# Performance work log

Hardware: AMD Instinct MI355X
Metric: run time of the kernel (lower is better)

Reference implementation:

```python
import jax, jax.numpy as jnp
import numpy as np

N_HEAD = 16
D_HEAD = 64
N_GROUPS = 4
D_EMBED = 1024
ROPE_N = 32
B, T = 2, 2048


def apply_rope(x, cos, sin):
    # x: (..., T, ROPE_N); cos/sin: (T, ROPE_N) broadcast over leading dims
    h = x.shape[-1]
    x1, x2 = x[..., : h // 2], x[..., h // 2 :]
    rotated = jnp.concatenate((-x2, x1), axis=-1)
    return (x * cos + rotated * sin).astype(x.dtype)


def setup_inputs() -> dict:
    key = jax.random.key(0)
    k1, k2, k3, k4, k5 = jax.random.split(key, 5)
    return {
        "x": jax.random.normal(k1, (B, T, D_EMBED), dtype=jnp.float32),
        "cos": jax.random.uniform(k2, (T, ROPE_N), dtype=jnp.float32),
        "sin": jax.random.uniform(k3, (T, ROPE_N), dtype=jnp.float32),
        "mask": jnp.ones((B, T), dtype=bool),  # unused by the original forward (passes None to SDPA)
        "Wqkv": jax.random.normal(k4, (D_EMBED, (N_HEAD + 2 * N_GROUPS) * D_HEAD), dtype=jnp.float32) * 0.02,
        "Wout": jax.random.normal(k5, (N_HEAD * D_HEAD, D_EMBED), dtype=jnp.float32) * 0.02,
    }


def reference(x, cos, sin, mask, Wqkv, Wout):
    Bv, Tv, _ = x.shape
    q_per_kv = N_HEAD // N_GROUPS  # 4
    total_qkv = q_per_kv + 2       # 6

    qkv = jnp.einsum("btc,cf->btf", x, Wqkv)  # (B, T, 1536)
    qkv = qkv.reshape(Bv, Tv, N_GROUPS, total_qkv, D_HEAD)
    qkv = jnp.transpose(qkv, (0, 2, 3, 1, 4))  # (B, G, total_qkv, T, d)

    q = qkv[:, :, :q_per_kv]           # (B, G, q_per_kv, T, d)
    k = qkv[:, :, q_per_kv : q_per_kv + 1]  # (B, G, 1, T, d)
    v = qkv[:, :, q_per_kv + 1 :]           # (B, G, 1, T, d)

    # GQA expand (1 < groups < heads)
    k = jnp.broadcast_to(k, (Bv, N_GROUPS, q_per_kv, Tv, D_HEAD))
    v = jnp.broadcast_to(v, (Bv, N_GROUPS, q_per_kv, Tv, D_HEAD))

    q = q.reshape(Bv, N_HEAD, Tv, D_HEAD)
    k = k.reshape(Bv, N_HEAD, Tv, D_HEAD)
    v = v.reshape(Bv, N_HEAD, Tv, D_HEAD)

    # partial RoPE on the first ROPE_N dims of each head
    q = jnp.concatenate((apply_rope(q[..., :ROPE_N], cos, sin), q[..., ROPE_N:]), axis=-1)
    k = jnp.concatenate((apply_rope(k[..., :ROPE_N], cos, sin), k[..., ROPE_N:]), axis=-1)

    scale = 1.0 / np.sqrt(D_HEAD).astype(np.float32)
    scores = jnp.einsum("bhtd,bhsd->bhts", q, k) * scale
    attn = jax.nn.softmax(scores, axis=-1)
    y = jnp.einsum("bhts,bhsd->bhtd", attn, v)   # (B, H, T, d)
    y = jnp.transpose(y, (0, 2, 1, 3)).reshape(Bv, Tv, N_HEAD * D_HEAD)
    return jnp.einsum("btf,fc->btc", y, Wout)
```

## Files before the change

kernel.cpp:

```cpp
#include <hip/hip_runtime.h>
#include <hip/hip_bf16.h>
#include <math.h>

#define BATCH   2
#define TSEQ    2048
#define DEMBED  1024
#define NHEAD   16
#define DHEAD   64
#define NGROUP  4
#define ROPEN   32
#define FQKV    1536
#define MROWS   (BATCH*TSEQ)

typedef __attribute__((ext_vector_type(8))) short short8;
typedef __attribute__((ext_vector_type(4))) float floatx4;

__device__ __forceinline__ void split_pack8(const float* f, uint4& h4, uint4& l4) {
    uint u[8], lu[8];
    #pragma unroll
    for (int j = 0; j < 8; ++j) {
        u[j] = __float_as_uint(f[j]);
        float lf = f[j] - __uint_as_float(u[j] & 0xffff0000u);
        lu[j] = __float_as_uint(lf);
    }
    h4.x = __builtin_amdgcn_perm(u[1], u[0], 0x07060302u);
    h4.y = __builtin_amdgcn_perm(u[3], u[2], 0x07060302u);
    h4.z = __builtin_amdgcn_perm(u[5], u[4], 0x07060302u);
    h4.w = __builtin_amdgcn_perm(u[7], u[6], 0x07060302u);
    l4.x = __builtin_amdgcn_perm(lu[1], lu[0], 0x07060302u);
    l4.y = __builtin_amdgcn_perm(lu[3], lu[2], 0x07060302u);
    l4.z = __builtin_amdgcn_perm(lu[5], lu[4], 0x07060302u);
    l4.w = __builtin_amdgcn_perm(lu[7], lu[6], 0x07060302u);
}

__device__ __forceinline__ void rtn_pack8(const float* f, uint4& h4) {
    uint t[8];
    #pragma unroll
    for (int j = 0; j < 8; ++j)
        t[j] = __float_as_uint(f[j]) + 0x8000u;
    h4.x = __builtin_amdgcn_perm(t[1], t[0], 0x07060302u);
    h4.y = __builtin_amdgcn_perm(t[3], t[2], 0x07060302u);
    h4.z = __builtin_amdgcn_perm(t[5], t[4], 0x07060302u);
    h4.w = __builtin_amdgcn_perm(t[7], t[6], 0x07060302u);
}

__device__ __forceinline__ uint pk_bf16x2(float f0, float f1) {
    uint u0 = __float_as_uint(f0) + 0x8000u;
    uint u1 = __float_as_uint(f1) + 0x8000u;
    return __builtin_amdgcn_perm(u1, u0, 0x07060302u);
}

__device__ __forceinline__ float fast_exp2(float x) {
    float r;
    asm("v_exp_f32 %0, %1" : "=v"(r) : "v"(x));
    return r;
}

__device__ __forceinline__ void lds_async16(void* lds, const void* gp) {
    __builtin_amdgcn_global_load_lds(
        (const __attribute__((address_space(1))) unsigned int*)gp,
        (__attribute__((address_space(3))) unsigned int*)lds,
        16, 0, 0);
}


__global__ __launch_bounds__(256) void conv_xy(const float* __restrict__ in,
                                               char* __restrict__ img) {
    const int tid = threadIdx.x;
    const int c   = blockIdx.x & 15;
    const int mt  = blockIdx.x >> 4;
    const int r    = tid >> 1;
    const int half = tid & 1;

    const float* src = in + (size_t)(mt*128 + r)*1024 + c*64 + half*32;
    float f[32];
    #pragma unroll
    for (int u = 0; u < 8; ++u)
        *(float4*)(f + 4*u) = *(const float4*)(src + 4*u);

    char* tile = img + ((size_t)(mt*16 + c)) * 32768;
    #pragma unroll
    for (int cc = 0; cc < 4; ++cc) {
        uint4 h4, l4;
        split_pack8(f + cc*8, h4, l4);
        int j    = half*4 + cc;
        int phys = j ^ (r & 7);
        *(uint4*)(tile + r*128 + phys*16)         = h4;
        *(uint4*)(tile + 16384 + r*128 + phys*16) = l4;
    }
}

__global__ __launch_bounds__(256) void conv_w(const float* __restrict__ W,
                                              int N,
                                              char* __restrict__ img) {
    __shared__ float Lf[64][132];
    const int tid = threadIdx.x;
    const int c   = blockIdx.x;
    const int nt  = blockIdx.y;

    {
        const int kk = tid >> 2;
        const int nc = (tid & 3) * 32;
        const float* src = W + (size_t)(c*64 + kk)*N + nt*128 + nc;
        #pragma unroll
        for (int u = 0; u < 8; ++u)
            *(float4*)(&Lf[kk][nc + 4*u]) = *(const float4*)(src + 4*u);
    }
    __syncthreads();

    char* tile = img + ((size_t)(nt*16 + c)) * 32768;
    #pragma unroll
    for (int rep = 0; rep < 4; ++rep) {
        int idx = rep*256 + tid;
        int n = idx & 127;
        int j = idx >> 7;
        float v[8];
        #pragma unroll
        for (int i = 0; i < 8; ++i) v[i] = Lf[j*8 + i][n];
        uint4 h4, l4;
        split_pack8(v, h4, l4);
        int phys = j ^ (n & 7);
        *(uint4*)(tile + n*128 + phys*16)         = h4;
        *(uint4*)(tile + 16384 + n*128 + phys*16) = l4;
    }
}

struct GemmAcc { floatx4 a[4][4]; };

__device__ __forceinline__ void gemm_mfma_core(const char* __restrict__ Aimg,
                                               const char* __restrict__ Bimg,
                                               char* smem, int mt, int nt,
                                               int tid, GemmAcc& G) {
    const int wv = tid >> 6;
    const int wm = wv & 1, wn = wv >> 1;
    const int lane = tid & 63;
    const int qd = lane >> 4, cl = lane & 15;
    const int wslot = (tid & 192) * 16;

    #pragma unroll
    for (int tm = 0; tm < 4; ++tm)
        #pragma unroll
        for (int tn = 0; tn < 4; ++tn)
            G.a[tm][tn] = (floatx4){0.f, 0.f, 0.f, 0.f};

    for (int c = 0; c < 16; ++c) {
        __syncthreads();
        {
            const uint4* gA = (const uint4*)(Aimg + ((size_t)(mt*16 + c)) * 32768) + tid;
            const uint4* gB = (const uint4*)(Bimg + ((size_t)(nt*16 + c)) * 32768) + tid;
            #pragma unroll
            for (int j = 0; j < 8; ++j) {
                lds_async16(smem + j*4096 + wslot,         gA + j*256);
                lds_async16(smem + 32768 + j*4096 + wslot, gB + j*256);
            }
        }
        __syncthreads();

        #pragma unroll
        for (int s = 0; s < 2; ++s) {
            const int phys = ((s*4 + qd) ^ (cl & 7)) * 16;
            short8 ah[4], al[4], bh[4], bl[4];
            #pragma unroll
            for (int tt = 0; tt < 4; ++tt) {
                const int rA = wm*64 + 16*tt + cl;
                ah[tt] = *(const short8*)(smem + rA*128 + phys);
                al[tt] = *(const short8*)(smem + 16384 + rA*128 + phys);
                const int rB = wn*64 + 16*tt + cl;
                bh[tt] = *(const short8*)(smem + 32768 + rB*128 + phys);
                bl[tt] = *(const short8*)(smem + 49152 + rB*128 + phys);
            }
            #pragma unroll
            for (int tm = 0; tm < 4; ++tm)
                #pragma unroll
                for (int tn = 0; tn < 4; ++tn) {
                    G.a[tm][tn] = __builtin_amdgcn_mfma_f32_16x16x32_bf16(ah[tm], bh[tn], G.a[tm][tn], 0, 0, 0);
                    G.a[tm][tn] = __builtin_amdgcn_mfma_f32_16x16x32_bf16(al[tm], bh[tn], G.a[tm][tn], 0, 0, 0);
                    G.a[tm][tn] = __builtin_amdgcn_mfma_f32_16x16x32_bf16(ah[tm], bl[tn], G.a[tm][tn], 0, 0, 0);
                }
        }
    }
}

__global__ __launch_bounds__(256, 2) void gemm_qkv_mfma(const char* __restrict__ Aimg,
                                                        const char* __restrict__ Bimg,
                                                        const float* __restrict__ cosp,
                                                        const float* __restrict__ sinp,
                                                        float* __restrict__ Qf,
                                                        ushort* __restrict__ Kimg,
                                                        ushort* __restrict__ Vimg) {
    __shared__ __align__(16) char smem[68608];
    const int tid = threadIdx.x;
    const int nt = blockIdx.x, mt = blockIdx.y;

    GemmAcc G;
    gemm_mfma_core(Aimg, Bimg, smem, mt, nt, tid, G);

    const int wv = tid >> 6;
    const int wm = wv & 1, wn = wv >> 1;
    const int lane = tid & 63;
    const int qd = lane >> 4, cl = lane & 15;

    const int slice = nt*2 + wn;
    const int g  = slice / 6;
    const int jj = slice % 6;
    const int b  = mt >> 4;

    if (jj != 5) {
        #pragma unroll
        for (int tm = 0; tm < 4; ++tm)
            #pragma unroll
            for (int r = 0; r < 4; ++r) {
                int m = mt*128 + wm*64 + 16*tm + 4*qd + r;
                int t = m & 2047;
                float c1 = cosp[t*ROPEN + cl],      s1 = sinp[t*ROPEN + cl];
                float c2 = cosp[t*ROPEN + 16 + cl], s2 = sinp[t*ROPEN + 16 + cl];
                float x1 = G.a[tm][0][r], x2 = G.a[tm][1][r];
                G.a[tm][0][r] = x1*c1 - x2*s1;
                G.a[tm][1][r] = x2*c2 + x1*s2;
            }
    }

    if (jj < 4) {
        #pragma unroll
        for (int tm = 0; tm < 4; ++tm)
            #pragma unroll
            for (int tn = 0; tn < 4; ++tn)
                #pragma unroll
                for (int r = 0; r < 4; ++r) {
                    int m = mt*128 + wm*64 + 16*tm + 4*qd + r;
                    Qf[(size_t)m*1024 + (g*4 + jj)*64 + 16*tn + cl] = G.a[tm][tn][r];
                }
    } else {
        float* Lw = (float*)(smem + wv*17152);
        __syncthreads();
        #pragma unroll
        for (int tm = 0; tm < 4; ++tm)
            #pragma unroll
            for (int tn = 0; tn < 4; ++tn)
                #pragma unroll
                for (int r = 0; r < 4; ++r)
                    Lw[(16*tm + 4*qd + r)*67 + 16*tn + cl] = G.a[tm][tn][r];
        __syncthreads();

        const int cloc = (mt & 15)*2 + wm;
        ushort* img = ((jj == 4) ? Kimg : Vimg)
                      + (size_t)(b*4 + g)*262144 + (size_t)cloc*8192;
        if (jj == 4) {
            const int rr = lane;
            float f[8];
            #pragma unroll
            for (int ch = 0; ch < 8; ++ch) {
                *(float4*)f       = *(const float4*)(&Lw[rr*67 + ch*8]);
                *(float4*)(f + 4) = *(const float4*)(&Lw[rr*67 + ch*8 + 4]);
                uint4 h4, l4;
                split_pack8(f, h4, l4);
                int phys = ch ^ (rr & 7);
                *(uint4*)(img + rr*64 + phys*8)        = h4;
                *(uint4*)(img + 4096 + rr*64 + phys*8) = l4;
            }
        } else {
            const int d = lane;
            float f[8];
            #pragma unroll
            for (int ch = 0; ch < 8; ++ch) {
                #pragma unroll
                for (int i = 0; i < 8; ++i) f[i] = Lw[(ch*8 + i)*67 + d];
                uint4 h4;
                rtn_pack8(f, h4);
                int phys = ch ^ (d & 7);
                *(uint4*)(img + d*64 + phys*8) = h4;
            }
        }
    }
}

__global__ __launch_bounds__(256, 2) void gemm_out_mfma(const char* __restrict__ Aimg,
                                                        const char* __restrict__ Bimg,
                                                        float* __restrict__ C) {
    __shared__ __align__(16) char smem[49152];
    const int tid = threadIdx.x;
    const int nt = blockIdx.x, mt = blockIdx.y;

    const int wv = tid >> 6;
    const int wm = wv & 1, wn = wv >> 1;
    const int lane = tid & 63;
    const int qd = lane >> 4, cl = lane & 15;
    const int wslot = (tid & 192) * 16;

    floatx4 acc[2][4];
    #pragma unroll
    for (int tm = 0; tm < 2; ++tm)
        #pragma unroll
        for (int tn = 0; tn < 4; ++tn)
            acc[tm][tn] = (floatx4){0.f, 0.f, 0.f, 0.f};

    for (int c = 0; c < 16; ++c) {
        __syncthreads();
        {
            const char* sA = Aimg + ((size_t)((mt >> 1)*16 + c))*32768
                                  + (mt & 1)*8192 + (size_t)tid*16;
            const char* sB = Bimg + ((size_t)(nt*16 + c))*32768 + (size_t)tid*16;
            lds_async16(smem + wslot,          sA);
            lds_async16(smem + 4096  + wslot,  sA + 4096);
            lds_async16(smem + 8192  + wslot,  sA + 16384);
            lds_async16(smem + 12288 + wslot,  sA + 16384 + 4096);
            #pragma unroll
            for (int j = 0; j < 4; ++j) {
                lds_async16(smem + 16384 + j*4096 + wslot, sB + j*4096);
                lds_async16(smem + 32768 + j*4096 + wslot, sB + 16384 + j*4096);
            }
        }
        __syncthreads();

        #pragma unroll
        for (int s = 0; s < 2; ++s) {
            const int phys = ((s*4 + qd) ^ (cl & 7)) * 16;
            short8 ah[2], al[2], bh[4], bl[4];
            #pragma unroll
            for (int tt = 0; tt < 2; ++tt) {
                const int rA = wm*32 + 16*tt + cl;
                ah[tt] = *(const short8*)(smem + rA*128 + phys);
                al[tt] = *(const short8*)(smem + 8192 + rA*128 + phys);
            }
            #pragma unroll
            for (int tt = 0; tt < 4; ++tt) {
                const int rB = wn*64 + 16*tt + cl;
                bh[tt] = *(const short8*)(smem + 16384 + rB*128 + phys);
                bl[tt] = *(const short8*)(smem + 32768 + rB*128 + phys);
            }
            #pragma unroll
            for (int tm = 0; tm < 2; ++tm)
                #pragma unroll
                for (int tn = 0; tn < 4; ++tn) {
                    acc[tm][tn] = __builtin_amdgcn_mfma_f32_16x16x32_bf16(ah[tm], bh[tn], acc[tm][tn], 0, 0, 0);
                    acc[tm][tn] = __builtin_amdgcn_mfma_f32_16x16x32_bf16(al[tm], bh[tn], acc[tm][tn], 0, 0, 0);
                    acc[tm][tn] = __builtin_amdgcn_mfma_f32_16x16x32_bf16(ah[tm], bl[tn], acc[tm][tn], 0, 0, 0);
                }
        }
    }

    #pragma unroll
    for (int tm = 0; tm < 2; ++tm)
        #pragma unroll
        for (int tn = 0; tn < 4; ++tn)
            #pragma unroll
            for (int r = 0; r < 4; ++r) {
                int m = mt*64 + wm*32 + 16*tm + 4*qd + r;
                int n = nt*128 + wn*64 + 16*tn + cl;
                C[(size_t)m*1024 + n] = acc[tm][tn][r];
            }
}

__global__ __launch_bounds__(256, 4) void attn10(const float* __restrict__ Qf,
                                                 const char* __restrict__ Kimg,
                                                 const char* __restrict__ Vimg,
                                                 char* __restrict__ Yimg) {
    __shared__ __align__(16) char smem[37888];
    uint* Pp32 = (uint*)(smem + 32768);

    const int tid  = threadIdx.x;
    const int wv   = tid >> 6;
    const int lane = tid & 63;
    const int qd   = lane >> 4;
    const int cl   = lane & 15;

    const int bg    = blockIdx.x & 7;
    const int inner = blockIdx.x >> 3;
    const int hj    = inner >> 5;
    const int qt    = inner & 31;
    const int b = bg >> 2, g = bg & 3;
    const int h = g*4 + hj;

    short8 qh[2], ql[2];
    {
        const float* qp = Qf + (size_t)(b*2048 + qt*64 + wv*16 + cl)*1024
                             + h*64 + 8*qd;
        #pragma unroll
        for (int s = 0; s < 2; ++s) {
            float f[8];
            *(float4*)f       = *(const float4*)(qp + 32*s);
            *(float4*)(f + 4) = *(const float4*)(qp + 32*s + 4);
            #pragma unroll
            for (int i = 0; i < 8; ++i) f[i] *= 0.125f * 1.44269504088896f;
            uint4 h4, l4;
            split_pack8(f, h4, l4);
            qh[s] = __builtin_bit_cast(short8, h4);
            ql[s] = __builtin_bit_cast(short8, l4);
        }
    }

    floatx4 accOT[4] = {};
    float lsum = 0.f;

    const char* Kg0 = Kimg + (size_t)bg*524288;
    const char* Vg0 = Vimg + (size_t)bg*524288;
    const int wslot = (tid & 192) * 16;

    {
        const char* src = Kg0 + (size_t)tid*16;
        #pragma unroll
        for (int j = 0; j < 4; ++j)
            lds_async16(smem + j*4096 + wslot, src + j*4096);
    }

    for (int c = 0; c < TSEQ/64; ++c) {
        __syncthreads();
        const int buf = c & 1;
        if (c + 1 < TSEQ/64) {
            const char* src = Kg0 + (size_t)(c+1)*16384 + (size_t)tid*16;
            #pragma unroll
            for (int j = 0; j < 4; ++j)
                lds_async16(smem + (1-buf)*16384 + j*4096 + wslot, src + j*4096);
        }
        const char* Kl = smem + buf*16384;
        const char* Vg = Vg0 + (size_t)c*16384;

        #pragma unroll
        for (int hh = 0; hh < 2; ++hh) {
            floatx4 accST[2] = {};
            __builtin_amdgcn_s_setprio(1);
            #pragma unroll
            for (int s = 0; s < 2; ++s) {
                #pragma unroll
                for (int tt = 0; tt < 2; ++tt) {
                    const int off = (32*hh + 16*tt + cl)*128
                                  + (((4*s + qd) ^ (cl & 7))*16);
                    short8 kh = *(const short8*)(Kl + off);
                    short8 kl = *(const short8*)(Kl + 8192 + off);
                    accST[tt] = __builtin_amdgcn_mfma_f32_16x16x32_bf16(kh, qh[s], accST[tt], 0, 0, 0);
                    accST[tt] = __builtin_amdgcn_mfma_f32_16x16x32_bf16(kh, ql[s], accST[tt], 0, 0, 0);
                    accST[tt] = __builtin_amdgcn_mfma_f32_16x16x32_bf16(kl, qh[s], accST[tt], 0, 0, 0);
                }
            }
            __builtin_amdgcn_s_setprio(0);

            float p[8];
            #pragma unroll
            for (int tt = 0; tt < 2; ++tt)
                #pragma unroll
                for (int r = 0; r < 4; ++r)
                    p[4*tt + r] = fast_exp2(accST[tt][r]);
            lsum += ((p[0] + p[1]) + (p[2] + p[3]))
                  + ((p[4] + p[5]) + (p[6] + p[7]));
            {
                uint* prow = Pp32 + (16*wv + cl)*20 + 2*qd;
                uint2 w0; w0.x = pk_bf16x2(p[0], p[1]); w0.y = pk_bf16x2(p[2], p[3]);
                uint2 w1; w1.x = pk_bf16x2(p[4], p[5]); w1.y = pk_bf16x2(p[6], p[7]);
                *(uint2*)(prow)     = w0;
                *(uint2*)(prow + 8) = w1;
            }

            uint4 paw = *(const uint4*)(Pp32 + (16*wv + cl)*20 + 4*qd);
            short8 pa = __builtin_bit_cast(short8, paw);
            __builtin_amdgcn_s_setprio(1);
            #pragma unroll
            for (int tt = 0; tt < 4; ++tt) {
                const int off = (16*tt + cl)*128 + (((4*hh + qd) ^ (cl & 7))*16);
                short8 vh = *(const short8*)(Vg + off);
                accOT[tt] = __builtin_amdgcn_mfma_f32_16x16x32_bf16(vh, pa, accOT[tt], 0, 0, 0);
            }
            __builtin_amdgcn_s_setprio(0);
        }
    }

    __syncthreads();
    float* Lt = (float*)smem;
    {
        float l = lsum;
        l += __shfl_xor(l, 16);
        l += __shfl_xor(l, 32);
        float inv = 1.0f / l;
        const int row = 16*wv + cl;
        #pragma unroll
        for (int tt = 0; tt < 4; ++tt)
            #pragma unroll
            for (int r = 0; r < 4; ++r)
                Lt[row*66 + 16*tt + 4*qd + r] = accOT[tt][r] * inv;
    }
    __syncthreads();
    {
        const int r0 = tid >> 2;
        const int qq = tid & 3;
        float f[16];
        #pragma unroll
        for (int u = 0; u < 8; ++u)
            *(float2*)(f + 2*u) = *(const float2*)(&Lt[r0*66 + qq*16 + 2*u]);
        const int R = (qt & 1)*64 + r0;
        char* tile = Yimg + (size_t)((b*16 + (qt >> 1))*16 + h) * 32768;
        #pragma unroll
        for (int cc = 0; cc < 2; ++cc) {
            uint4 h4, l4;
            split_pack8(f + 8*cc, h4, l4);
            int j    = qq*2 + cc;
            int phys = j ^ (R & 7);
            *(uint4*)(tile + R*128 + phys*16)         = h4;
            *(uint4*)(tile + 16384 + R*128 + phys*16) = l4;
        }
    }
}

extern "C" void kernel_launch(void* const* d_in, const int* in_sizes, int n_in,
                              void* d_out, int out_size, void* d_ws, size_t ws_size,
                              hipStream_t stream) {
    const float* x    = (const float*)d_in[0];
    const float* cosp = (const float*)d_in[1];
    const float* sinp = (const float*)d_in[2];
    const float* Wqkv = (const float*)d_in[4];
    const float* Wout = (const float*)d_in[5];
    float* out = (float*)d_out;

    char* ws = (char*)d_ws;
    float*  Qf    = (float*)(ws);
    ushort* Kimg  = (ushort*)(ws + ((size_t)16<<20));
    ushort* Vimg  = (ushort*)(ws + ((size_t)20<<20));
    char*   Bo    = ws + ((size_t)24<<20);
    char*   Ximg  = ws + ((size_t)28<<20);
    char*   Bq    = ws + ((size_t)44<<20);
    char*   Yimg  = ws + ((size_t)28<<20);

    conv_xy<<<512, 256, 0, stream>>>(x, Ximg);
    conv_w<<<dim3(16, 12), 256, 0, stream>>>(Wqkv, FQKV, Bq);
    conv_w<<<dim3(16, 8), 256, 0, stream>>>(Wout, DEMBED, Bo);
    gemm_qkv_mfma<<<dim3(12, 32), 256, 0, stream>>>(Ximg, Bq, cosp, sinp,
                                                    Qf, Kimg, Vimg);
    attn10<<<1024, 256, 0, stream>>>(Qf, (const char*)Kimg, (const char*)Vimg,
                                     Yimg);
    gemm_out_mfma<<<dim3(8, 64), 256, 0, stream>>>(Yimg, Bo, out);
}
```

Before: 241.0 us.

## Permute V image k-order so P stays in registers for PV MFMA

The V-image packing in the conversion kernel now interleaves key indices so the layout of each lane's exp-score accumulator lines up with the B-operand layout the PV MFMA expects. This removes the LDS round trip used to transpose P (write packed bf16, then read back) and frees the 5 KB P scratch buffer. The V loads for each half-chunk are also hoisted ahead of the QK^T MFMAs so global latency overlaps compute. Correctness depends on the permutation in the converter matching the accumulator-to-operand mapping exactly.

```diff
diff --git a/kernel.cpp b/kernel.cpp
--- a/kernel.cpp
+++ b/kernel.cpp
@@ -263,8 +263,11 @@
             float f[8];
             #pragma unroll
             for (int ch = 0; ch < 8; ++ch) {
-                #pragma unroll
-                for (int i = 0; i < 8; ++i) f[i] = Lw[(ch*8 + i)*67 + d];
+                const int kb = 32*(ch >> 2) + 4*(ch & 3);
+                #pragma unroll
+                for (int i = 0; i < 4; ++i) f[i]     = Lw[(kb + i)*67 + d];
+                #pragma unroll
+                for (int i = 0; i < 4; ++i) f[4 + i] = Lw[(kb + 16 + i)*67 + d];
                 uint4 h4;
                 rtn_pack8(f, h4);
                 int phys = ch ^ (d & 7);
@@ -351,12 +354,11 @@
             }
 }
 
-__global__ __launch_bounds__(256, 4) void attn10(const float* __restrict__ Qf,
+__global__ __launch_bounds__(256, 4) void attn11(const float* __restrict__ Qf,
                                                  const char* __restrict__ Kimg,
                                                  const char* __restrict__ Vimg,
                                                  char* __restrict__ Yimg) {
-    __shared__ __align__(16) char smem[37888];
-    uint* Pp32 = (uint*)(smem + 32768);
+    __shared__ __align__(16) char smem[32768];
 
     const int tid  = threadIdx.x;
     const int wv   = tid >> 6;
@@ -396,6 +398,13 @@
     const char* Vg0 = Vimg + (size_t)bg*524288;
     const int wslot = (tid & 192) * 16;
 
+    int voff[2][4];
+    #pragma unroll
+    for (int hh = 0; hh < 2; ++hh)
+        #pragma unroll
+        for (int tt = 0; tt < 4; ++tt)
+            voff[hh][tt] = (16*tt + cl)*128 + (((4*hh + qd) ^ (cl & 7))*16);
+
     {
         const char* src = Kg0 + (size_t)tid*16;
         #pragma unroll
@@ -417,6 +426,11 @@
 
         #pragma unroll
         for (int hh = 0; hh < 2; ++hh) {
+            short8 vh[4];
+            #pragma unroll
+            for (int tt = 0; tt < 4; ++tt)
+                vh[tt] = *(const short8*)(Vg + voff[hh][tt]);
+
             floatx4 accST[2] = {};
             __builtin_amdgcn_s_setprio(1);
             #pragma unroll
@@ -442,23 +456,17 @@
                     p[4*tt + r] = fast_exp2(accST[tt][r]);
             lsum += ((p[0] + p[1]) + (p[2] + p[3]))
                   + ((p[4] + p[5]) + (p[6] + p[7]));
-            {
-                uint* prow = Pp32 + (16*wv + cl)*20 + 2*qd;
-                uint2 w0; w0.x = pk_bf16x2(p[0], p[1]); w0.y = pk_bf16x2(p[2], p[3]);
-                uint2 w1; w1.x = pk_bf16x2(p[4], p[5]); w1.y = pk_bf16x2(p[6], p[7]);
-                *(uint2*)(prow)     = w0;
-                *(uint2*)(prow + 8) = w1;
-            }
-
-            uint4 paw = *(const uint4*)(Pp32 + (16*wv + cl)*20 + 4*qd);
+            uint4 paw;
+            paw.x = pk_bf16x2(p[0], p[1]);
+            paw.y = pk_bf16x2(p[2], p[3]);
+            paw.z = pk_bf16x2(p[4], p[5]);
+            paw.w = pk_bf16x2(p[6], p[7]);
             short8 pa = __builtin_bit_cast(short8, paw);
+
             __builtin_amdgcn_s_setprio(1);
             #pragma unroll
-            for (int tt = 0; tt < 4; ++tt) {
-                const int off = (16*tt + cl)*128 + (((4*hh + qd) ^ (cl & 7))*16);
-                short8 vh = *(const short8*)(Vg + off);
-                accOT[tt] = __builtin_amdgcn_mfma_f32_16x16x32_bf16(vh, pa, accOT[tt], 0, 0, 0);
-            }
+            for (int tt = 0; tt < 4; ++tt)
+                accOT[tt] = __builtin_amdgcn_mfma_f32_16x16x32_bf16(vh[tt], pa, accOT[tt], 0, 0, 0);
             __builtin_amdgcn_s_setprio(0);
         }
     }
@@ -523,7 +531,7 @@
     conv_w<<<dim3(16, 8), 256, 0, stream>>>(Wout, DEMBED, Bo);
     gemm_qkv_mfma<<<dim3(12, 32), 256, 0, stream>>>(Ximg, Bq, cosp, sinp,
                                                     Qf, Kimg, Vimg);
-    attn10<<<1024, 256, 0, stream>>>(Qf, (const char*)Kimg, (const char*)Vimg,
+    attn11<<<1024, 256, 0, stream>>>(Qf, (const char*)Kimg, (const char*)Vimg,
                                      Yimg);
     gemm_out_mfma<<<dim3(8, 64), 256, 0, stream>>>(Yimg, Bo, out);
 }
```

After: 243.4 us. About the same (+1.0%).
